# Kernel optimization log

Measured on AMD Instinct MI355X. Metric: run time of the kernel, lower is better.

The kernel has to match this reference:

```python
import jax, jax.numpy as jnp
import numpy as np

B_, L_, D_MODEL, N_LAYER, VOCAB = 4, 2048, 512, 2, 128
D_INNER, D_STATE, DT_RANK, D_CONV = 2 * D_MODEL, 16, D_MODEL // 16, 4
NDIR = 2  # forward / backward Mamba stacks


def setup_inputs() -> dict:
    key = jax.random.key(0)
    ks = jax.random.split(key, 12)
    f = jax.random.normal
    A_init = jnp.broadcast_to(
        jnp.log(jnp.arange(1, D_STATE + 1, dtype=jnp.float32)),
        (NDIR, N_LAYER, D_INNER, D_STATE)) + 0.0
    return {
        "input_ids": jax.random.randint(ks[0], (B_, L_), 0, VOCAB),
        "padding_mask": jnp.ones((B_, L_), dtype=bool),
        "embed": 0.02 * f(ks[1], (NDIR, VOCAB, D_MODEL)),
        "in_proj_w": 0.02 * f(ks[2], (NDIR, N_LAYER, 2 * D_INNER, D_MODEL)),
        "conv_w": 0.1 * f(ks[3], (NDIR, N_LAYER, D_INNER, 1, D_CONV)),
        "conv_b": 0.1 * f(ks[4], (NDIR, N_LAYER, D_INNER)),
        "x_proj_w": 0.02 * f(ks[5], (NDIR, N_LAYER, DT_RANK + 2 * D_STATE, D_INNER)),
        "dt_proj_w": 0.1 * f(ks[6], (NDIR, N_LAYER, D_INNER, DT_RANK)),
        "dt_proj_b": -4.0 + 0.5 * jax.random.uniform(ks[7], (NDIR, N_LAYER, D_INNER)),
        "A_log": A_init,
        "D": jnp.ones((NDIR, N_LAYER, D_INNER)),
        "out_proj_w": 0.02 * f(ks[8], (NDIR, N_LAYER, D_MODEL, D_INNER)),
        "norm_w": jnp.ones((NDIR, N_LAYER, D_MODEL)),
        "norm_f_w": jnp.ones((NDIR, D_MODEL)),
        "proj_w": 0.02 * f(ks[9], (D_MODEL, 2 * D_MODEL)),
        "proj_b": jnp.zeros((D_MODEL,)),
    }


def _rmsnorm(x, w, eps=1e-5):
    return x * jax.lax.rsqrt(jnp.mean(jnp.square(x), axis=-1, keepdims=True) + eps) * w


def _selective_scan(u, dt, Bm, Cm, A, Dp):
    # u, dt: (b, l, d_inner); Bm, Cm: (b, l, d_state)
    b, l, di = u.shape

    def step(h, inp):
        u_t, dt_t, b_t, c_t = inp                      # (b,di) (b,di) (b,n) (b,n)
        dA = jnp.exp(dt_t[:, :, None] * A)             # (b, di, n)
        h = dA * h + (dt_t * u_t)[:, :, None] * b_t[:, None, :]
        return h, jnp.einsum('bdn,bn->bd', h, c_t)

    h0 = jnp.zeros((b, di, A.shape[-1]), u.dtype)
    xs = (jnp.swapaxes(u, 0, 1), jnp.swapaxes(dt, 0, 1),
          jnp.swapaxes(Bm, 0, 1), jnp.swapaxes(Cm, 0, 1))
    _, ys = jax.lax.scan(step, h0, xs)                 # ys: (l, b, di)
    return jnp.swapaxes(ys, 0, 1) + u * Dp


def _mamba(x, p):
    in_w, cw, cb, xw, dtw, dtb, alog, dp, ow = p
    xz = jnp.einsum('bld,ed->ble', x, in_w)            # (b, l, 2*d_inner)
    u, z = jnp.split(xz, 2, axis=-1)
    uc = jnp.swapaxes(u, 1, 2)                         # (b, d_inner, l)
    uc = jax.lax.conv_general_dilated(
        uc, cw, (1,), [(D_CONV - 1, 0)], feature_group_count=D_INNER)
    u = jax.nn.silu(jnp.swapaxes(uc + cb[None, :, None], 1, 2))
    xdbl = jnp.einsum('bld,ed->ble', u, xw)
    dt, Bm, Cm = jnp.split(xdbl, [DT_RANK, DT_RANK + D_STATE], axis=-1)
    dt = jax.nn.softplus(jnp.einsum('blr,dr->bld', dt, dtw) + dtb)
    y = _selective_scan(u, dt, Bm, Cm, -jnp.exp(alog), dp)
    y = y * jax.nn.silu(z)
    return jnp.einsum('bld,ed->ble', y, ow)


def _mixer(ids, d, embed, in_proj_w, conv_w, conv_b, x_proj_w, dt_proj_w,
           dt_proj_b, A_log, D, out_proj_w, norm_w, norm_f_w):
    hidden = embed[d][ids]
    residual = None
    for i in range(N_LAYER):
        residual = hidden if residual is None else hidden + residual
        hidden = _rmsnorm(residual, norm_w[d, i])
        p = (in_proj_w[d, i], conv_w[d, i], conv_b[d, i], x_proj_w[d, i],
             dt_proj_w[d, i], dt_proj_b[d, i], A_log[d, i], D[d, i],
             out_proj_w[d, i])
        hidden = _mamba(hidden, p)
    return _rmsnorm(hidden + residual, norm_f_w[d])


def reference(input_ids, padding_mask, embed, in_proj_w, conv_w, conv_b,
              x_proj_w, dt_proj_w, dt_proj_b, A_log, D, out_proj_w, norm_w,
              norm_f_w, proj_w, proj_b):
    args = (embed, in_proj_w, conv_w, conv_b, x_proj_w, dt_proj_w, dt_proj_b,
            A_log, D, out_proj_w, norm_w, norm_f_w)
    fwd = _mixer(input_ids, 0, *args)
    bwd = jnp.flip(_mixer(jnp.flip(input_ids, 1), 1, *args), 1)
    out = jnp.concatenate([fwd, bwd], axis=-1)        # (b, l, 2*d_model)
    return jnp.einsum('ble,oe->blo', out, proj_w) + proj_b
```

## Files before the change

kernel.cpp:

```cpp
#include <hip/hip_runtime.h>
#include <hip/hip_bf16.h>

#define B_   4
#define L_   2048
#define DM   512
#define DI   1024
#define NST  16
#define DTR  32
#define ROWS (B_ * L_)
#define NCHUNK 64
#define CLEN  (L_ / NCHUNK)
#define LN2R 1.4426950408889634f

typedef unsigned short u16;
typedef __attribute__((ext_vector_type(8))) short bf16x8;
typedef __attribute__((ext_vector_type(4))) float f32x4;
typedef __attribute__((ext_vector_type(4))) float float4v;
typedef __attribute__((ext_vector_type(2))) float f32x2;

__device__ __forceinline__ float bf2f(u16 h) {
  union { unsigned int u; float f; } v; v.u = ((unsigned int)h) << 16; return v.f;
}
__device__ __forceinline__ u16 f2bf(float f) {
  union { float f; unsigned int u; } v; v.f = f;
  unsigned int u = v.u;
  if ((u & 0x7fffffffu) > 0x7f800000u) return (u16)((u >> 16) | 0x0040u);
  return (u16)((u + 0x7fffu + ((u >> 16) & 1u)) >> 16);
}
__device__ __forceinline__ float sigmoidf_(float x) { return 1.f / (1.f + __expf(-x)); }

__device__ __forceinline__ f32x2 pk_mul(f32x2 a, f32x2 b) {
  f32x2 d; asm("v_pk_mul_f32 %0, %1, %2" : "=v"(d) : "v"(a), "v"(b)); return d;
}
__device__ __forceinline__ f32x2 pk_fma(f32x2 a, f32x2 b, f32x2 c) {
  f32x2 d; asm("v_pk_fma_f32 %0, %1, %2, %3" : "=v"(d) : "v"(a), "v"(b), "v"(c)); return d;
}

__device__ __forceinline__ void gload16(const u16* g, u16* l) {
  __builtin_amdgcn_global_load_lds(
      (const __attribute__((address_space(1))) void*)g,
      (__attribute__((address_space(3))) void*)l, 16, 0, 0);
}

__global__ __launch_bounds__(256) void cvt_k(const float* __restrict__ in,
                                             u16* __restrict__ out, int n4) {
  int i = blockIdx.x * 256 + threadIdx.x;
  if (i >= n4) return;
  float4v v = *(const float4v*)&in[i * 4];
  u16 o[4];
  o[0] = f2bf(v.x); o[1] = f2bf(v.y); o[2] = f2bf(v.z); o[3] = f2bf(v.w);
  *(ulong1*)&out[i * 4] = *(ulong1*)o;
}

__global__ __launch_bounds__(256) void trp_k(const float* __restrict__ in,
                                             float* __restrict__ out) {
  int o = blockIdx.x * 256 + threadIdx.x;
  int li = o >> 15;
  int k = (o >> 10) & (DTR - 1);
  int d = o & (DI - 1);
  out[o] = in[((size_t)li * DI + d) * DTR + k];
}

__global__ __launch_bounds__(256) void embed_k(const int* __restrict__ ids,
                                               const float* __restrict__ emb,
                                               float* __restrict__ res, int flip) {
  int idx = blockIdx.x * 256 + threadIdx.x;
  int c = idx & (DM - 1);
  int row = idx >> 9;
  int b = row >> 11;
  int l = row & (L_ - 1);
  int sl = flip ? (L_ - 1 - l) : l;
  int id = ids[(b << 11) + sl];
  res[idx] = emb[id * DM + c];
}

template <bool ADD>
__global__ __launch_bounds__(256) void addnorm_k(float* __restrict__ res,
                                                 const float* __restrict__ hid,
                                                 const float* __restrict__ w,
                                                 u16* __restrict__ xn) {
  int row = blockIdx.x;
  int tid = threadIdx.x;
  int base = row * DM;
  float x0 = res[base + tid];
  float x1 = res[base + 256 + tid];
  if (ADD) {
    x0 += hid[base + tid];
    x1 += hid[base + 256 + tid];
    res[base + tid] = x0;
    res[base + 256 + tid] = x1;
  }
  float s = x0 * x0 + x1 * x1;
  for (int off = 32; off; off >>= 1) s += __shfl_xor(s, off);
  __shared__ float ps[4];
  if (!(tid & 63)) ps[tid >> 6] = s;
  __syncthreads();
  float tot = ps[0] + ps[1] + ps[2] + ps[3];
  float rs = 1.f / sqrtf(tot / (float)DM + 1e-5f);
  xn[base + tid]       = f2bf(x0 * rs * w[tid]);
  xn[base + 256 + tid] = f2bf(x1 * rs * w[tid + 256]);
}

__global__ __launch_bounds__(512) void gemm256_k(const u16* __restrict__ A,
                                                 const u16* __restrict__ W,
                                                 u16* __restrict__ outp,
                                                 int N, int K) {
  constexpr int BK = 32;
  __shared__ u16 As[3][256 * BK];
  __shared__ u16 Wsh[3][256 * BK];
  int tid = threadIdx.x;
  int lane = tid & 63;
  int wv = tid >> 6;
  int wr = wv >> 2, wc = wv & 3;
  int bid = blockIdx.x;
  int xcd = bid & 7, jj = bid >> 3;
  int mt = (xcd & 3) * 8 + (jj & 7);
  int nt = (xcd >> 2) * 4 + (jj >> 3);
  int m0 = mt * 256, n0 = nt * 256;
  f32x4 acc[8][4];
#pragma unroll
  for (int i = 0; i < 8; ++i)
#pragma unroll
    for (int j = 0; j < 4; ++j) acc[i][j] = (f32x4){0.f, 0.f, 0.f, 0.f};
  int rr = lane & 15;
  int kk = (lane >> 4) << 3;
  int l4 = lane >> 2;
  int c8 = (lane & 3) << 3;
  const u16* Ag = A + (size_t)(m0 + l4) * K + c8;
  const u16* Wg = W + (size_t)(n0 + l4) * K + c8;

  auto stage = [&](int k0, int buf) {
    gload16(Ag + (size_t)(wv * 16) * K + k0, &As[buf][wv * 512]);
    gload16(Ag + (size_t)((wv + 8) * 16) * K + k0, &As[buf][(wv + 8) * 512]);
    gload16(Wg + (size_t)(wv * 16) * K + k0, &Wsh[buf][wv * 512]);
    gload16(Wg + (size_t)((wv + 8) * 16) * K + k0, &Wsh[buf][(wv + 8) * 512]);
  };

  int NK = K / BK;
  stage(0, 0); stage(BK, 1);
  for (int k = 0; k < NK; ++k) {
    if (k < NK - 1)
      asm volatile("s_waitcnt vmcnt(4)" ::: "memory");
    else
      asm volatile("s_waitcnt vmcnt(0)" ::: "memory");
    __builtin_amdgcn_s_barrier();
    __builtin_amdgcn_sched_barrier(0);
    if (k + 2 < NK) stage((k + 2) * BK, (k + 2) % 3);
    __builtin_amdgcn_sched_barrier(0);
    int cur = k % 3;
    bf16x8 af[8], wf[4];
#pragma unroll
    for (int mi = 0; mi < 8; ++mi)
      af[mi] = *(bf16x8*)&As[cur][(wr * 128 + mi * 16 + rr) * BK + kk];
#pragma unroll
    for (int ni = 0; ni < 4; ++ni)
      wf[ni] = *(bf16x8*)&Wsh[cur][(wc * 64 + ni * 16 + rr) * BK + kk];
#pragma unroll
    for (int mi = 0; mi < 8; ++mi)
#pragma unroll
      for (int ni = 0; ni < 4; ++ni)
        acc[mi][ni] = __builtin_amdgcn_mfma_f32_16x16x32_bf16(af[mi], wf[ni], acc[mi][ni], 0, 0, 0);
  }
  int cr = (lane >> 4) << 2;
  int cc = lane & 15;
#pragma unroll
  for (int mi = 0; mi < 8; ++mi)
#pragma unroll
    for (int ni = 0; ni < 4; ++ni) {
      int row = m0 + wr * 128 + mi * 16 + cr;
      int col = n0 + wc * 64 + ni * 16 + cc;
#pragma unroll
      for (int j = 0; j < 4; ++j)
        outp[(size_t)(row + j) * N + col] = f2bf(acc[mi][ni][j]);
    }
}

#define EPI_F32  0
#define EPI_BF16 1
#define EPI_BIAS 2

template <int BN, int EPI, int SK = 1>
__global__ __launch_bounds__(256) void gemm_bt(const u16* __restrict__ A,
                                               const u16* __restrict__ W,
                                               void* __restrict__ outp,
                                               const float* __restrict__ bias,
                                               int N, int K) {
  constexpr int BM = 128, BK = 32;
  constexpr int NF = BN / 32;
  constexpr int G = (BN == 128) ? 4 : 3;
  __shared__ u16 As[4][BM * BK];
  __shared__ u16 Wsh[4][BN * BK];
  int tid = threadIdx.x;
  int lane = tid & 63;
  int wv = tid >> 6;
  int wr = wv >> 1, wc = wv & 1;
  int m0 = blockIdx.x * BM;
  int n0 = (SK > 1) ? 0 : blockIdx.y * BN;
  int koff = (SK > 1) ? blockIdx.y * (K / SK) : 0;
  int KS = K / SK;
  int NK = KS / BK;
  f32x4 acc[4][NF];
#pragma unroll
  for (int i = 0; i < 4; ++i)
#pragma unroll
    for (int j = 0; j < NF; ++j) acc[i][j] = (f32x4){0.f, 0.f, 0.f, 0.f};
  int rr = lane & 15;
  int kk = (lane >> 4) << 3;
  int l4 = lane >> 2;
  int c8 = (lane & 3) << 3;
  const u16* Ag = A + (size_t)(m0 + l4) * K + koff + c8;
  const u16* Wg = W + (size_t)(n0 + l4) * K + koff + c8;

  auto stage = [&](int k0, int buf) {
    gload16(Ag + (size_t)(wv * 16) * K + k0, &As[buf][wv * 512]);
    gload16(Ag + (size_t)((wv + 4) * 16) * K + k0, &As[buf][(wv + 4) * 512]);
    gload16(Wg + (size_t)(wv * 16) * K + k0, &Wsh[buf][wv * 512]);
    if (BN == 128)
      gload16(Wg + (size_t)((wv + 4) * 16) * K + k0, &Wsh[buf][(wv + 4) * 512]);
  };

  stage(0, 0); stage(BK, 1); stage(2 * BK, 2);
  for (int k = 0; k < NK; ++k) {
    if (k < NK - 2)
      asm volatile("s_waitcnt vmcnt(%0)" :: "n"(2 * G) : "memory");
    else if (k == NK - 2)
      asm volatile("s_waitcnt vmcnt(%0)" :: "n"(G) : "memory");
    else
      asm volatile("s_waitcnt vmcnt(0)" ::: "memory");
    __builtin_amdgcn_s_barrier();
    __builtin_amdgcn_sched_barrier(0);
    if (k + 3 < NK) stage((k + 3) * BK, (k + 3) & 3);
    __builtin_amdgcn_sched_barrier(0);
    int cur = k & 3;
    bf16x8 af[4], wf[NF];
#pragma unroll
    for (int mi = 0; mi < 4; ++mi)
      af[mi] = *(bf16x8*)&As[cur][(wr * 64 + mi * 16 + rr) * BK + kk];
#pragma unroll
    for (int ni = 0; ni < NF; ++ni)
      wf[ni] = *(bf16x8*)&Wsh[cur][(wc * (BN / 2) + ni * 16 + rr) * BK + kk];
#pragma unroll
    for (int mi = 0; mi < 4; ++mi)
#pragma unroll
      for (int ni = 0; ni < NF; ++ni)
        acc[mi][ni] = __builtin_amdgcn_mfma_f32_16x16x32_bf16(af[mi], wf[ni], acc[mi][ni], 0, 0, 0);
  }
  int cr = (lane >> 4) << 2;
  int cc = lane & 15;
  float* outF = (float*)outp + ((SK > 1) ? (size_t)blockIdx.y * (size_t)ROWS * N : 0);
#pragma unroll
  for (int mi = 0; mi < 4; ++mi)
#pragma unroll
    for (int ni = 0; ni < NF; ++ni) {
      int row = m0 + wr * 64 + mi * 16 + cr;
      int col = n0 + wc * (BN / 2) + ni * 16 + cc;
      float bv = (EPI == EPI_BIAS) ? bias[col] : 0.f;
#pragma unroll
      for (int j = 0; j < 4; ++j) {
        float v = acc[mi][ni][j] + bv;
        if (EPI == EPI_BF16)
          ((u16*)outp)[(size_t)(row + j) * N + col] = f2bf(v);
        else
          outF[(size_t)(row + j) * N + col] = v;
      }
    }
}

__global__ __launch_bounds__(256) void conv_k(const u16* __restrict__ xz,
                                              const float* __restrict__ cw,
                                              const float* __restrict__ cb,
                                              u16* __restrict__ uh) {
  int idx = blockIdx.x * 256 + threadIdx.x;
  int c = idx & (DI - 1);
  int row = idx >> 10;
  int l = row & (L_ - 1);
  float acc = cb[c];
#pragma unroll
  for (int j = 0; j < 4; ++j) {
    int ls = l + j - 3;
    if (ls >= 0)
      acc += bf2f(xz[(size_t)(row + j - 3) * (2 * DI) + c]) * cw[c * 4 + j];
  }
  float s = acc * sigmoidf_(acc);
  uh[idx] = f2bf(s);
}

__device__ __forceinline__ bool a_fast(const float* alog, int d, float& a20) {
  a20 = -__expf(alog[d * NST]) * LN2R;
  bool fast = true;
#pragma unroll
  for (int n = 1; n < NST; ++n) {
    float an = -__expf(alog[d * NST + n]) * LN2R;
    fast &= (fabsf(an - (float)(n + 1) * a20) <= 1e-5f * (float)(n + 1) * fabsf(a20));
  }
  return fast;
}

__device__ __forceinline__ void stage_xs(float (*xs)[64], const float* xp,
                                         int b, int t0, int tid) {
  size_t base = ((size_t)b * L_ + t0) * 64;
  const float4v* s0 = (const float4v*)(xp + base);
  const float4v* s1 = (const float4v*)(xp + (size_t)ROWS * 64 + base);
  const float4v* s2 = (const float4v*)(xp + (size_t)2 * ROWS * 64 + base);
  const float4v* s3 = (const float4v*)(xp + (size_t)3 * ROWS * 64 + base);
  float4v* dst = (float4v*)&xs[0][0];
  dst[tid]       = s0[tid]       + s1[tid]       + s2[tid]       + s3[tid];
  dst[tid + 256] = s0[tid + 256] + s1[tid + 256] + s2[tid + 256] + s3[tid + 256];
}

__global__ __launch_bounds__(256) void dtscan1_k(const u16* __restrict__ uh,
                                                 const float* __restrict__ xp,
                                                 const float* __restrict__ dtw_t,
                                                 const float* __restrict__ dtb,
                                                 const float* __restrict__ alog,
                                                 float* __restrict__ dtf,
                                                 float* __restrict__ chk) {
  __shared__ float xs[CLEN][64];
  int blk = blockIdx.x;
  int db = blk & 3;
  int c  = (blk >> 2) & (NCHUNK - 1);
  int b  = blk >> 8;
  int tid = threadIdx.x;
  int d  = db * 256 + tid;
  int t0 = c * CLEN;
  stage_xs(xs, xp, b, t0, tid);
  f32x2 w2[16];
#pragma unroll
  for (int j = 0; j < 16; ++j)
    w2[j] = (f32x2){dtw_t[(size_t)(2 * j) * DI + d], dtw_t[(size_t)(2 * j + 1) * DI + d]};
  float bias = dtb[d];
  float a20;
  bool fast = a_fast(alog, d, a20);
  __syncthreads();
  float S = 0.f;
  size_t ubase = ((size_t)b * L_ + t0) * DI + d;
  f32x2 h2[8];
#pragma unroll
  for (int q = 0; q < 8; ++q) h2[q] = (f32x2){0.f, 0.f};
  for (int t = 0; t < CLEN; ++t) {
    f32x2 a2 = {bias, 0.f};
    const f32x2* xr2 = (const f32x2*)&xs[t][0];
#pragma unroll
    for (int j = 0; j < 16; ++j) a2 = pk_fma(xr2[j], w2[j], a2);
    float a = a2.x + a2.y;
    float dtv = (a > 15.f) ? a : __logf(1.f + __expf(a));
    dtf[ubase] = dtv;
    float du = dtv * bf2f(uh[ubase]);
    S += dtv;
    if (fast) {
      float p1 = exp2f(dtv * a20);
      float p2 = p1 * p1;
      f32x2 pw = {p1, p2};
      f32x2 pst = {p2, p2};
      f32x2 du2 = {du, du};
#pragma unroll
      for (int k = 0; k < 4; ++k) {
        f32x4 bv = *(const f32x4*)&xs[t][DTR + k * 4];
        f32x2 blo = __builtin_shufflevector(bv, bv, 0, 1);
        f32x2 bhi = __builtin_shufflevector(bv, bv, 2, 3);
        h2[2 * k]     = pk_fma(pw, h2[2 * k], pk_mul(du2, blo));
        pw = pk_mul(pw, pst);
        h2[2 * k + 1] = pk_fma(pw, h2[2 * k + 1], pk_mul(du2, bhi));
        if (k < 3) pw = pk_mul(pw, pst);
      }
    } else {
#pragma unroll
      for (int q = 0; q < 8; ++q) {
        float e0 = exp2f(dtv * -__expf(alog[d * NST + 2 * q]) * LN2R);
        float e1 = exp2f(dtv * -__expf(alog[d * NST + 2 * q + 1]) * LN2R);
        f32x2 bv = *(const f32x2*)&xs[t][DTR + q * 2];
        h2[q] = pk_fma((f32x2){e0, e1}, h2[q], pk_mul((f32x2){du, du}, bv));
      }
    }
    ubase += DI;
  }
  const size_t H = (size_t)B_ * NCHUNK * DI * NST;
  size_t idx = ((size_t)(b * NCHUNK + c) * DI + d) * NST;
#pragma unroll
  for (int n = 0; n < NST; ++n) {
    float an = -__expf(alog[d * NST + n]) * LN2R;
    chk[idx + n]     = exp2f(an * S);
    chk[H + idx + n] = (n & 1) ? h2[n >> 1].y : h2[n >> 1].x;
  }
}

__global__ __launch_bounds__(256) void scan2_k(float* __restrict__ chk) {
  int j = blockIdx.x * 256 + threadIdx.x;
  int n = j & 15;
  int d = (j >> 4) & (DI - 1);
  int b = j >> 14;
  const size_t H = (size_t)B_ * NCHUNK * DI * NST;
  float h = 0.f;
  for (int c = 0; c < NCHUNK; ++c) {
    size_t idx = ((size_t)(b * NCHUNK + c) * DI + d) * NST + n;
    float a = chk[idx];
    float hl = chk[H + idx];
    chk[H + idx] = h;
    h = a * h + hl;
  }
}

__global__ __launch_bounds__(256) void scan3_k(const u16* __restrict__ uh,
                                               const float* __restrict__ dtf,
                                               const float* __restrict__ xp,
                                               const float* __restrict__ alog,
                                               const float* __restrict__ dvec,
                                               const float* __restrict__ chk,
                                               const u16* __restrict__ xz,
                                               u16* __restrict__ yg) {
  __shared__ float xs[CLEN][64];
  int blk = blockIdx.x;
  int db = blk & 3;
  int c  = (blk >> 2) & (NCHUNK - 1);
  int b  = blk >> 8;
  int tid = threadIdx.x;
  int d  = db * 256 + tid;
  int t0 = c * CLEN;
  stage_xs(xs, xp, b, t0, tid);
  float a20;
  bool fast = a_fast(alog, d, a20);
  const size_t H = (size_t)B_ * NCHUNK * DI * NST;
  size_t cidx = ((size_t)(b * NCHUNK + c) * DI + d) * NST;
  f32x2 h2[8];
#pragma unroll
  for (int q = 0; q < 8; ++q) h2[q] = *(const f32x2*)&chk[H + cidx + 2 * q];
  float Dv = dvec[d];
  __syncthreads();
  size_t ubase = ((size_t)b * L_ + t0) * DI + d;
  size_t zbase = ((size_t)b * L_ + t0) * (2 * DI) + DI + d;
  if (fast) {
    for (int t = 0; t < CLEN; ++t) {
      float dtv = dtf[ubase];
      float uv  = bf2f(uh[ubase]);
      float du  = dtv * uv;
      float p1 = exp2f(dtv * a20);
      float p2 = p1 * p1;
      f32x2 pw = {p1, p2};
      f32x2 pst = {p2, p2};
      f32x2 du2 = {du, du};
      f32x2 acc2 = {0.f, 0.f};
#pragma unroll
      for (int k = 0; k < 4; ++k) {
        f32x4 bv = *(const f32x4*)&xs[t][DTR + k * 4];
        f32x4 cv = *(const f32x4*)&xs[t][DTR + NST + k * 4];
        f32x2 blo = __builtin_shufflevector(bv, bv, 0, 1);
        f32x2 bhi = __builtin_shufflevector(bv, bv, 2, 3);
        f32x2 clo = __builtin_shufflevector(cv, cv, 0, 1);
        f32x2 chi = __builtin_shufflevector(cv, cv, 2, 3);
        h2[2 * k]     = pk_fma(pw, h2[2 * k], pk_mul(du2, blo));
        acc2          = pk_fma(h2[2 * k], clo, acc2);
        pw = pk_mul(pw, pst);
        h2[2 * k + 1] = pk_fma(pw, h2[2 * k + 1], pk_mul(du2, bhi));
        acc2          = pk_fma(h2[2 * k + 1], chi, acc2);
        if (k < 3) pw = pk_mul(pw, pst);
      }
      float y = acc2.x + acc2.y + uv * Dv;
      float z = bf2f(xz[zbase]);
      yg[ubase] = f2bf(y * z * sigmoidf_(z));
      ubase += DI; zbase += 2 * DI;
    }
  } else {
    float A2[NST];
#pragma unroll
    for (int n = 0; n < NST; ++n) A2[n] = -__expf(alog[d * NST + n]) * LN2R;
    for (int t = 0; t < CLEN; ++t) {
      float dtv = dtf[ubase];
      float uv  = bf2f(uh[ubase]);
      float du  = dtv * uv;
      f32x2 acc2 = {0.f, 0.f};
#pragma unroll
      for (int q = 0; q < 8; ++q) {
        f32x2 bv = *(const f32x2*)&xs[t][DTR + q * 2];
        f32x2 cv = *(const f32x2*)&xs[t][DTR + NST + q * 2];
        f32x2 e = {exp2f(dtv * A2[2 * q]), exp2f(dtv * A2[2 * q + 1])};
        h2[q] = pk_fma(e, h2[q], pk_mul((f32x2){du, du}, bv));
        acc2 = pk_fma(h2[q], cv, acc2);
      }
      float y = acc2.x + acc2.y + uv * Dv;
      float z = bf2f(xz[zbase]);
      yg[ubase] = f2bf(y * z * sigmoidf_(z));
      ubase += DI; zbase += 2 * DI;
    }
  }
}

__global__ __launch_bounds__(256) void fincat_k(const float* __restrict__ hid,
                                                const float* __restrict__ res,
                                                const float* __restrict__ w,
                                                u16* __restrict__ cat, int dir) {
  int row = blockIdx.x;
  int tid = threadIdx.x;
  int base = row * DM;
  float x0 = hid[base + tid] + res[base + tid];
  float x1 = hid[base + 256 + tid] + res[base + 256 + tid];
  float s = x0 * x0 + x1 * x1;
  for (int off = 32; off; off >>= 1) s += __shfl_xor(s, off);
  __shared__ float ps[4];
  if (!(tid & 63)) ps[tid >> 6] = s;
  __syncthreads();
  float tot = ps[0] + ps[1] + ps[2] + ps[3];
  float rs = 1.f / sqrtf(tot / (float)DM + 1e-5f);
  int b = row >> 11, l = row & (L_ - 1);
  size_t drow = dir ? ((size_t)(b << 11) + (L_ - 1 - l)) : (size_t)row;
  size_t obase = drow * (2 * DM) + (size_t)dir * DM;
  cat[obase + tid]       = f2bf(x0 * rs * w[tid]);
  cat[obase + 256 + tid] = f2bf(x1 * rs * w[tid + 256]);
}

extern "C" void kernel_launch(void* const* d_in, const int* in_sizes, int n_in,
                              void* d_out, int out_size, void* d_ws, size_t ws_size,
                              hipStream_t stream) {
  const int*   ids      = (const int*)d_in[0];
  const float* embed    = (const float*)d_in[2];
  const float* in_w     = (const float*)d_in[3];
  const float* conv_w   = (const float*)d_in[4];
  const float* conv_b   = (const float*)d_in[5];
  const float* x_w      = (const float*)d_in[6];
  const float* dt_w     = (const float*)d_in[7];
  const float* dt_bias  = (const float*)d_in[8];
  const float* A_log    = (const float*)d_in[9];
  const float* Dp       = (const float*)d_in[10];
  const float* out_w    = (const float*)d_in[11];
  const float* norm_w   = (const float*)d_in[12];
  const float* norm_f   = (const float*)d_in[13];
  const float* proj_w   = (const float*)d_in[14];
  const float* proj_b   = (const float*)d_in[15];

  char* ws = (char*)d_ws;
  size_t off = 0;
  auto alloc = [&](size_t bytes) {
    void* p = ws + off;
    off += (bytes + 255) & ~(size_t)255;
    return p;
  };
  float* res  = (float*)alloc((size_t)ROWS * DM * 4);
  float* hid  = (float*)alloc((size_t)ROWS * DM * 4);
  u16*   xnyg = (u16*)alloc((size_t)ROWS * DI * 2);
  u16*   xz   = (u16*)alloc((size_t)ROWS * 2 * DI * 2);
  u16*   u_h  = (u16*)alloc((size_t)ROWS * DI * 2);
  float* dtf  = (float*)alloc((size_t)ROWS * DI * 4);
  float* chk  = (float*)alloc((size_t)2 * B_ * NCHUNK * DI * NST * 4);
  u16*   cat  = (u16*)alloc((size_t)ROWS * 2 * DM * 2);
  const int N_IN  = 4 * 2 * DI * DM;
  const int N_XW  = 4 * 64 * DI;
  const int N_OW  = 4 * DM * DI;
  const int N_PW  = DM * 2 * DM;
  const int N_DTW = 4 * DTR * DI;
  u16*   in_wb  = (u16*)alloc((size_t)N_IN * 2);
  u16*   x_wb   = (u16*)alloc((size_t)N_XW * 2);
  u16*   out_wb = (u16*)alloc((size_t)N_OW * 2);
  u16*   pr_wb  = (u16*)alloc((size_t)N_PW * 2);
  float* dtw_t  = (float*)alloc((size_t)N_DTW * 4);
  if (off > ws_size) return;

  cvt_k<<<(N_IN / 4 + 255) / 256, 256, 0, stream>>>(in_w, in_wb, N_IN / 4);
  cvt_k<<<(N_XW / 4 + 255) / 256, 256, 0, stream>>>(x_w, x_wb, N_XW / 4);
  cvt_k<<<(N_OW / 4 + 255) / 256, 256, 0, stream>>>(out_w, out_wb, N_OW / 4);
  cvt_k<<<(N_PW / 4 + 255) / 256, 256, 0, stream>>>(proj_w, pr_wb, N_PW / 4);
  trp_k<<<N_DTW / 256, 256, 0, stream>>>(dt_w, dtw_t);

  for (int d = 0; d < 2; ++d) {
    embed_k<<<ROWS * DM / 256, 256, 0, stream>>>(ids, embed + (size_t)d * 128 * DM, res, d);
    for (int i = 0; i < 2; ++i) {
      int li = d * 2 + i;
      if (i == 0)
        addnorm_k<false><<<ROWS, 256, 0, stream>>>(res, hid, norm_w + (size_t)li * DM, xnyg);
      else
        addnorm_k<true><<<ROWS, 256, 0, stream>>>(res, hid, norm_w + (size_t)li * DM, xnyg);
      gemm256_k<<<256, 512, 0, stream>>>(
          xnyg, in_wb + (size_t)li * 2 * DI * DM, xz, 2 * DI, DM);
      conv_k<<<ROWS * DI / 256, 256, 0, stream>>>(
          xz, conv_w + (size_t)li * DI * 4, conv_b + (size_t)li * DI, u_h);
      gemm_bt<64, EPI_F32, 4><<<dim3(ROWS / 128, 4), 256, 0, stream>>>(
          u_h, x_wb + (size_t)li * 64 * DI, hid, nullptr, 64, DI);
      dtscan1_k<<<B_ * NCHUNK * (DI / 256), 256, 0, stream>>>(
          u_h, hid, dtw_t + (size_t)li * DTR * DI, dt_bias + (size_t)li * DI,
          A_log + (size_t)li * DI * NST, dtf, chk);
      scan2_k<<<(B_ * DI * NST) / 256, 256, 0, stream>>>(chk);
      scan3_k<<<B_ * NCHUNK * (DI / 256), 256, 0, stream>>>(
          u_h, dtf, hid, A_log + (size_t)li * DI * NST, Dp + (size_t)li * DI, chk,
          xz, xnyg);
      gemm_bt<64, EPI_F32><<<dim3(ROWS / 128, DM / 64), 256, 0, stream>>>(
          xnyg, out_wb + (size_t)li * DM * DI, hid, nullptr, DM, DI);
    }
    fincat_k<<<ROWS, 256, 0, stream>>>(hid, res, norm_f + (size_t)d * DM, cat, d);
  }
  gemm_bt<64, EPI_BIAS><<<dim3(ROWS / 128, DM / 64), 256, 0, stream>>>(
      cat, pr_wb, (float*)d_out, proj_b, DM, DI);
}
```

Baseline: 842.7 us.

## Rewrite in_proj GEMM as 8-phase ping-pong pipeline with swizzled LDS

```diff
diff --git a/kernel.cpp b/kernel.cpp
--- a/kernel.cpp
+++ b/kernel.cpp
@@ -101,13 +101,14 @@
   xn[base + 256 + tid] = f2bf(x1 * rs * w[tid + 256]);
 }
 
-__global__ __launch_bounds__(512) void gemm256_k(const u16* __restrict__ A,
-                                                 const u16* __restrict__ W,
-                                                 u16* __restrict__ outp,
-                                                 int N, int K) {
-  constexpr int BK = 32;
-  __shared__ u16 As[3][256 * BK];
-  __shared__ u16 Wsh[3][256 * BK];
+#define MFMA_B16(a, b, c) __builtin_amdgcn_mfma_f32_16x16x32_bf16(a, b, c, 0, 0, 0)
+
+__global__ __launch_bounds__(512) void gemm8p_k(const u16* __restrict__ A,
+                                                const u16* __restrict__ W,
+                                                u16* __restrict__ outp,
+                                                int N, int K) {
+  __shared__ u16 As[2][2][256 * 32];
+  __shared__ u16 Wsh[2][2][256 * 32];
   int tid = threadIdx.x;
   int lane = tid & 63;
   int wv = tid >> 6;
@@ -123,43 +124,115 @@
 #pragma unroll
     for (int j = 0; j < 4; ++j) acc[i][j] = (f32x4){0.f, 0.f, 0.f, 0.f};
   int rr = lane & 15;
-  int kk = (lane >> 4) << 3;
-  int l4 = lane >> 2;
-  int c8 = (lane & 3) << 3;
-  const u16* Ag = A + (size_t)(m0 + l4) * K + c8;
-  const u16* Wg = W + (size_t)(n0 + l4) * K + c8;
-
-  auto stage = [&](int k0, int buf) {
-    gload16(Ag + (size_t)(wv * 16) * K + k0, &As[buf][wv * 512]);
-    gload16(Ag + (size_t)((wv + 8) * 16) * K + k0, &As[buf][(wv + 8) * 512]);
-    gload16(Wg + (size_t)(wv * 16) * K + k0, &Wsh[buf][wv * 512]);
-    gload16(Wg + (size_t)((wv + 8) * 16) * K + k0, &Wsh[buf][(wv + 8) * 512]);
+  int sl = lane >> 4;
+  int pofs = ((sl + (rr >> 1)) & 3) * 8;
+  int lr = lane >> 2;
+  int ls = ((lane & 3) - (lr >> 1)) & 3;
+
+  auto stA = [&](int tau, int ks) {
+    int buf = tau & 1;
+#pragma unroll
+    for (int j = 0; j < 2; ++j)
+      gload16(A + (size_t)(m0 + j * 128 + wv * 16 + lr) * K + tau * 64 + ks * 32 + ls * 8,
+              &As[buf][ks][(j * 128 + wv * 16) * 32]);
   };
-
-  int NK = K / BK;
-  stage(0, 0); stage(BK, 1);
-  for (int k = 0; k < NK; ++k) {
-    if (k < NK - 1)
+  auto stW = [&](int tau, int ks) {
+    int buf = tau & 1;
+#pragma unroll
+    for (int j = 0; j < 2; ++j)
+      gload16(W + (size_t)(n0 + j * 128 + wv * 16 + lr) * K + tau * 64 + ks * 32 + ls * 8,
+              &Wsh[buf][ks][(j * 128 + wv * 16) * 32]);
+  };
+
+  int NT = K / 64;
+  stA(0, 0); stW(0, 0); stA(0, 1); stW(0, 1);
+  asm volatile("s_waitcnt vmcnt(4)" ::: "memory");
+  __builtin_amdgcn_sched_barrier(0);
+  __builtin_amdgcn_s_barrier();
+  __builtin_amdgcn_sched_barrier(0);
+
+  for (int tau = 0; tau < NT; ++tau) {
+    int buf = tau & 1;
+    bool more = (tau + 1 < NT);
+    bf16x8 af[8], w0, w1;
+#pragma unroll
+    for (int mi = 0; mi < 8; ++mi)
+      af[mi] = *(bf16x8*)&As[buf][0][(wr * 128 + mi * 16 + rr) * 32 + pofs];
+    w0 = *(bf16x8*)&Wsh[buf][0][(wc * 64 + 0 * 16 + rr) * 32 + pofs];
+    w1 = *(bf16x8*)&Wsh[buf][0][(wc * 64 + 1 * 16 + rr) * 32 + pofs];
+    if (more) stA(tau + 1, 0);
+    __builtin_amdgcn_sched_barrier(0);
+    __builtin_amdgcn_s_barrier();
+    asm volatile("s_waitcnt lgkmcnt(0)" ::: "memory");
+    __builtin_amdgcn_sched_barrier(0);
+    __builtin_amdgcn_s_setprio(1);
+#pragma unroll
+    for (int mi = 0; mi < 8; ++mi) {
+      acc[mi][0] = MFMA_B16(af[mi], w0, acc[mi][0]);
+      acc[mi][1] = MFMA_B16(af[mi], w1, acc[mi][1]);
+    }
+    __builtin_amdgcn_s_setprio(0);
+    __builtin_amdgcn_s_barrier();
+    __builtin_amdgcn_sched_barrier(0);
+    w0 = *(bf16x8*)&Wsh[buf][0][(wc * 64 + 2 * 16 + rr) * 32 + pofs];
+    w1 = *(bf16x8*)&Wsh[buf][0][(wc * 64 + 3 * 16 + rr) * 32 + pofs];
+    if (more) {
+      stW(tau + 1, 0);
       asm volatile("s_waitcnt vmcnt(4)" ::: "memory");
-    else
+    } else {
       asm volatile("s_waitcnt vmcnt(0)" ::: "memory");
-    __builtin_amdgcn_s_barrier();
-    __builtin_amdgcn_sched_barrier(0);
-    if (k + 2 < NK) stage((k + 2) * BK, (k + 2) % 3);
-    __builtin_amdgcn_sched_barrier(0);
-    int cur = k % 3;
-    bf16x8 af[8], wf[4];
+    }
+    __builtin_amdgcn_sched_barrier(0);
+    __builtin_amdgcn_s_barrier();
+    asm volatile("s_waitcnt lgkmcnt(0)" ::: "memory");
+    __builtin_amdgcn_sched_barrier(0);
+    __builtin_amdgcn_s_setprio(1);
+#pragma unroll
+    for (int mi = 0; mi < 8; ++mi) {
+      acc[mi][2] = MFMA_B16(af[mi], w0, acc[mi][2]);
+      acc[mi][3] = MFMA_B16(af[mi], w1, acc[mi][3]);
+    }
+    __builtin_amdgcn_s_setprio(0);
+    __builtin_amdgcn_s_barrier();
+    __builtin_amdgcn_sched_barrier(0);
 #pragma unroll
     for (int mi = 0; mi < 8; ++mi)
-      af[mi] = *(bf16x8*)&As[cur][(wr * 128 + mi * 16 + rr) * BK + kk];
-#pragma unroll
-    for (int ni = 0; ni < 4; ++ni)
-      wf[ni] = *(bf16x8*)&Wsh[cur][(wc * 64 + ni * 16 + rr) * BK + kk];
-#pragma unroll
-    for (int mi = 0; mi < 8; ++mi)
-#pragma unroll
-      for (int ni = 0; ni < 4; ++ni)
-        acc[mi][ni] = __builtin_amdgcn_mfma_f32_16x16x32_bf16(af[mi], wf[ni], acc[mi][ni], 0, 0, 0);
+      af[mi] = *(bf16x8*)&As[buf][1][(wr * 128 + mi * 16 + rr) * 32 + pofs];
+    w0 = *(bf16x8*)&Wsh[buf][1][(wc * 64 + 0 * 16 + rr) * 32 + pofs];
+    w1 = *(bf16x8*)&Wsh[buf][1][(wc * 64 + 1 * 16 + rr) * 32 + pofs];
+    if (more) stA(tau + 1, 1);
+    __builtin_amdgcn_sched_barrier(0);
+    __builtin_amdgcn_s_barrier();
+    asm volatile("s_waitcnt lgkmcnt(0)" ::: "memory");
+    __builtin_amdgcn_sched_barrier(0);
+    __builtin_amdgcn_s_setprio(1);
+#pragma unroll
+    for (int mi = 0; mi < 8; ++mi) {
+      acc[mi][0] = MFMA_B16(af[mi], w0, acc[mi][0]);
+      acc[mi][1] = MFMA_B16(af[mi], w1, acc[mi][1]);
+    }
+    __builtin_amdgcn_s_setprio(0);
+    __builtin_amdgcn_s_barrier();
+    __builtin_amdgcn_sched_barrier(0);
+    w0 = *(bf16x8*)&Wsh[buf][1][(wc * 64 + 2 * 16 + rr) * 32 + pofs];
+    w1 = *(bf16x8*)&Wsh[buf][1][(wc * 64 + 3 * 16 + rr) * 32 + pofs];
+    if (more) {
+      stW(tau + 1, 1);
+      asm volatile("s_waitcnt vmcnt(4)" ::: "memory");
+    }
+    __builtin_amdgcn_sched_barrier(0);
+    __builtin_amdgcn_s_barrier();
+    asm volatile("s_waitcnt lgkmcnt(0)" ::: "memory");
+    __builtin_amdgcn_sched_barrier(0);
+    __builtin_amdgcn_s_setprio(1);
+#pragma unroll
+    for (int mi = 0; mi < 8; ++mi) {
+      acc[mi][2] = MFMA_B16(af[mi], w0, acc[mi][2]);
+      acc[mi][3] = MFMA_B16(af[mi], w1, acc[mi][3]);
+    }
+    __builtin_amdgcn_s_setprio(0);
+    __builtin_amdgcn_s_barrier();
+    __builtin_amdgcn_sched_barrier(0);
   }
   int cr = (lane >> 4) << 2;
   int cc = lane & 15;
@@ -567,7 +640,7 @@
         addnorm_k<false><<<ROWS, 256, 0, stream>>>(res, hid, norm_w + (size_t)li * DM, xnyg);
       else
         addnorm_k<true><<<ROWS, 256, 0, stream>>>(res, hid, norm_w + (size_t)li * DM, xnyg);
-      gemm256_k<<<256, 512, 0, stream>>>(
+      gemm8p_k<<<256, 512, 0, stream>>>(
           xnyg, in_wb + (size_t)li * 2 * DI * DM, xz, 2 * DI, DM);
       conv_k<<<ROWS * DI / 256, 256, 0, stream>>>(
           xz, conv_w + (size_t)li * DI * 4, conv_b + (size_t)li * DI, u_h);
```

Result: faster. 823.3 us (-2.3%).
